# Kernel optimization log

Hardware: AMD Instinct MI355X
Metric: run time of the kernel (lower is better)

## Reference

```python
import jax, jax.numpy as jnp
import numpy as np

B, CIN, H, W = 8, 1, 192, 192
COUT, KH, KW = 8, 7, 7


def setup_inputs() -> dict:
    key = jax.random.key(0)
    k1, k2, k3 = jax.random.split(key, 3)
    x = jax.random.normal(k1, (B, CIN, H, W), dtype=jnp.float32)
    # original init: filter ~ N(0, 0.01), alpha = 0 (use small nonzero alpha)
    filt = 0.01 * jax.random.normal(k2, (COUT, CIN, KH, KW), dtype=jnp.float32)
    alpha = 0.1 * jax.random.normal(k3, (COUT, CIN), dtype=jnp.float32)
    return {"x": x, "filt": filt, "alpha": alpha}


def _smorph(x, filt, alpha):
    # x: [B, Cin, H, W]; filt: [Cout, Cin, kh, kw]; alpha: [Cout, Cin]
    b, cin, h, w = x.shape
    cout, _, kh, kw = filt.shape
    ho, wo = h - kh + 1, w - kw + 1  # 'valid' windowing as in _smorph_py
    # sliding-window patches: [B, Cin, kh*kw, Ho, Wo] (static slices, traced once)
    patches = jnp.stack(
        [x[:, :, ky:ky + ho, kx:kx + wo] for ky in range(kh) for kx in range(kw)],
        axis=2,
    )
    # s[b,co,ci,k,y,x] = input[b,ci,y+ky,x+kx] + filter[co,ci,ky,kx]
    s = patches[:, None] + filt.reshape(cout, cin, kh * kw, 1, 1)[None]
    a = alpha[None, :, :, None, None, None]  # broadcast over B, taps, space
    e = jnp.exp(a * s)
    num = jnp.sum(s * e, axis=(2, 3))  # sum over Cin and taps -> [B,Cout,Ho,Wo]
    den = jnp.sum(e, axis=(2, 3))
    return num / den


def reference(x, filt, alpha):
    # dual=False: single soft-morphology pass
    return _smorph(x, filt, alpha)
```

## Files before the change

### kernel.cpp

```cpp
#include <hip/hip_runtime.h>

#ifndef __has_builtin
#define __has_builtin(x) 0
#endif

__device__ __forceinline__ float fexp2(float v) {
#if __has_builtin(__builtin_amdgcn_exp2f)
    return __builtin_amdgcn_exp2f(v);
#else
    return exp2f(v);
#endif
}
__device__ __forceinline__ float frcp(float v) {
#if __has_builtin(__builtin_amdgcn_rcpf)
    return __builtin_amdgcn_rcpf(v);
#else
    return 1.0f / v;
#endif
}

constexpr int B_    = 8;
constexpr int H_    = 192;
constexpr int W_    = 192;
constexpr int COUT_ = 8;
constexpr int KH_   = 7;
constexpr int KW_   = 7;
constexpr int HO_   = H_ - KH_ + 1;
constexpr int WO_   = W_ - KW_ + 1;
constexpr float LOG2E = 1.44269504088896340736f;

constexpr int TX   = 64;
constexpr int TY   = 8;
constexpr int IX   = TX + KW_ - 1;
constexpr int IY   = TY + KH_ - 1;
constexpr int NPIX = IX * IY;

__global__ void smorph_setup(const float* __restrict__ filt,
                             const float* __restrict__ alpha,
                             float* __restrict__ ws) {
    int i = threadIdx.x;
    if (i < COUT_ * KH_) {
        int c = i / 7, ky = i - c * 7;
        float a2 = alpha[c] * LOG2E;
        float* t = ws + (c * 7 + ky) * 16;
#pragma unroll
        for (int kx = 0; kx < 7; ++kx) {
            float f = filt[(c * 7 + ky) * 7 + kx];
            float F = fexp2(a2 * f);
            t[kx]     = F;
            t[8 + kx] = F * f;
        }
        t[7] = 0.f; t[15] = 0.f;
    }
}

__global__ __launch_bounds__(256) void smorph_main(
    const float* __restrict__ x,
    const float* __restrict__ alpha,
    const float* __restrict__ fg,
    float* __restrict__ out)
{
    __shared__ __align__(16) float2 PH[IY * IX];

    const int tx  = threadIdx.x;
    const int ty  = threadIdx.y;
    const int tid = ty * 32 + tx;
    const int bx0 = blockIdx.x * TX;
    const int by0 = blockIdx.y * TY;
    const int z   = blockIdx.z;
    const int c   = z & 7;
    const float* xb = x + (z >> 3) * (H_ * W_);
    const float a2  = alpha[c] * LOG2E;

    const int i0 = tid, i1 = tid + 256, i2 = tid + 512, i3 = tid + 768;
    const int iy0 = i0 / IX, ix0 = i0 - iy0 * IX;
    const int iy1 = i1 / IX, ix1 = i1 - iy1 * IX;
    const int iy2 = i2 / IX, ix2 = i2 - iy2 * IX;
    const int iy3 = i3 / IX, ix3 = i3 - iy3 * IX;
    const bool has3 = (i3 < NPIX);

    const float xv0 = xb[min(by0 + iy0, H_ - 1) * W_ + min(bx0 + ix0, W_ - 1)];
    const float xv1 = xb[min(by0 + iy1, H_ - 1) * W_ + min(bx0 + ix1, W_ - 1)];
    const float xv2 = xb[min(by0 + iy2, H_ - 1) * W_ + min(bx0 + ix2, W_ - 1)];
    const float xv3 = has3 ? xb[min(by0 + iy3, H_ - 1) * W_ + min(bx0 + ix3, W_ - 1)] : 0.f;

    {
        float P;
        P = fexp2(a2 * xv0); PH[iy0 * IX + ix0] = make_float2(P, xv0 * P);
        P = fexp2(a2 * xv1); PH[iy1 * IX + ix1] = make_float2(P, xv1 * P);
        P = fexp2(a2 * xv2); PH[iy2 * IX + ix2] = make_float2(P, xv2 * P);
        if (has3) { P = fexp2(a2 * xv3); PH[iy3 * IX + ix3] = make_float2(P, xv3 * P); }
    }
    __syncthreads();

    const int ox = bx0 + 2 * tx;
    const int oy = by0 + ty;
    const bool valid = (ox + 1 < WO_) && (oy < HO_);

    float num0 = 0.f, den0 = 0.f, num1 = 0.f, den1 = 0.f;
    const float* tc = fg + c * (7 * 16);
#pragma unroll
    for (int ky = 0; ky < KH_; ++ky) {
        const float* t = tc + ky * 16;
        const float4* rp = (const float4*)&PH[(ty + ky) * IX + 2 * tx];
        float4 q0 = rp[0], q1 = rp[1], q2 = rp[2], q3 = rp[3];
        float P[8]  = {q0.x, q0.z, q1.x, q1.z, q2.x, q2.z, q3.x, q3.z};
        float Hh[8] = {q0.y, q0.w, q1.y, q1.w, q2.y, q2.w, q3.y, q3.w};
#pragma unroll
        for (int kx = 0; kx < 7; ++kx) {
            const float F = t[kx], G = t[8 + kx];
            num0 = fmaf(F, Hh[kx],     num0);
            num0 = fmaf(G, P[kx],      num0);
            den0 = fmaf(F, P[kx],      den0);
            num1 = fmaf(F, Hh[kx + 1], num1);
            num1 = fmaf(G, P[kx + 1],  num1);
            den1 = fmaf(F, P[kx + 1],  den1);
        }
    }

    if (valid) {
        float2 o;
        o.x = num0 * frcp(den0);
        o.y = num1 * frcp(den1);
        *(float2*)&out[(z * HO_ + oy) * WO_ + ox] = o;
    }
}

extern "C" void kernel_launch(void* const* d_in, const int* in_sizes, int n_in,
                              void* d_out, int out_size, void* d_ws, size_t ws_size,
                              hipStream_t stream) {
    const float* x     = (const float*)d_in[0];
    const float* filt  = (const float*)d_in[1];
    const float* alpha = (const float*)d_in[2];
    float* out = (float*)d_out;
    float* ws  = (float*)d_ws;

    smorph_setup<<<1, 64, 0, stream>>>(filt, alpha, ws);

    dim3 block(32, 8, 1);
    dim3 grid((WO_ + TX - 1) / TX, (HO_ + TY - 1) / TY, B_ * COUT_);
    smorph_main<<<grid, block, 0, stream>>>(x, alpha, ws, out);
}
```

Baseline: 73.98 us.

## Compute four output rows per thread with taller tiles to reuse LDS row loads

Raises the tile height from 8 to 32 rows so each thread computes a 4x2 output patch. Each shared-memory row is read once and applied to up to four output rows, which cuts LDS reads per output and shrinks the halo overhead per tile. In exchange it needs more registers for the accumulators and larger shared memory. It also launches fewer blocks, and the last row tile is partly wasted because 186 rows do not divide evenly by 32.

```diff
diff --git a/kernel.cpp b/kernel.cpp
--- a/kernel.cpp
+++ b/kernel.cpp
@@ -30,10 +30,11 @@
 constexpr float LOG2E = 1.44269504088896340736f;
 
 constexpr int TX   = 64;
-constexpr int TY   = 8;
+constexpr int TY   = 32;
 constexpr int IX   = TX + KW_ - 1;
 constexpr int IY   = TY + KH_ - 1;
 constexpr int NPIX = IX * IY;
+constexpr int NSLOT = (NPIX + 255) / 256;
 
 __global__ void smorph_setup(const float* __restrict__ filt,
                              const float* __restrict__ alpha,
@@ -72,57 +73,59 @@
     const float* xb = x + (z >> 3) * (H_ * W_);
     const float a2  = alpha[c] * LOG2E;
 
-    const int i0 = tid, i1 = tid + 256, i2 = tid + 512, i3 = tid + 768;
-    const int iy0 = i0 / IX, ix0 = i0 - iy0 * IX;
-    const int iy1 = i1 / IX, ix1 = i1 - iy1 * IX;
-    const int iy2 = i2 / IX, ix2 = i2 - iy2 * IX;
-    const int iy3 = i3 / IX, ix3 = i3 - iy3 * IX;
-    const bool has3 = (i3 < NPIX);
-
-    const float xv0 = xb[min(by0 + iy0, H_ - 1) * W_ + min(bx0 + ix0, W_ - 1)];
-    const float xv1 = xb[min(by0 + iy1, H_ - 1) * W_ + min(bx0 + ix1, W_ - 1)];
-    const float xv2 = xb[min(by0 + iy2, H_ - 1) * W_ + min(bx0 + ix2, W_ - 1)];
-    const float xv3 = has3 ? xb[min(by0 + iy3, H_ - 1) * W_ + min(bx0 + ix3, W_ - 1)] : 0.f;
-
-    {
-        float P;
-        P = fexp2(a2 * xv0); PH[iy0 * IX + ix0] = make_float2(P, xv0 * P);
-        P = fexp2(a2 * xv1); PH[iy1 * IX + ix1] = make_float2(P, xv1 * P);
-        P = fexp2(a2 * xv2); PH[iy2 * IX + ix2] = make_float2(P, xv2 * P);
-        if (has3) { P = fexp2(a2 * xv3); PH[iy3 * IX + ix3] = make_float2(P, xv3 * P); }
+#pragma unroll
+    for (int s = 0; s < NSLOT; ++s) {
+        const int i = tid + 256 * s;
+        if (i < NPIX) {
+            const int iy = i / IX, ix = i - iy * IX;
+            const float xv = xb[min(by0 + iy, H_ - 1) * W_ + min(bx0 + ix, W_ - 1)];
+            const float P = fexp2(a2 * xv);
+            PH[i] = make_float2(P, xv * P);
+        }
     }
     __syncthreads();
 
-    const int ox = bx0 + 2 * tx;
-    const int oy = by0 + ty;
-    const bool valid = (ox + 1 < WO_) && (oy < HO_);
+    const int ox  = bx0 + 2 * tx;
+    const int oyb = by0 + 4 * ty;
+    const bool vx = (ox + 1 < WO_);
 
-    float num0 = 0.f, den0 = 0.f, num1 = 0.f, den1 = 0.f;
+    float num[4][2] = {};
+    float den[4][2] = {};
     const float* tc = fg + c * (7 * 16);
+
 #pragma unroll
-    for (int ky = 0; ky < KH_; ++ky) {
-        const float* t = tc + ky * 16;
-        const float4* rp = (const float4*)&PH[(ty + ky) * IX + 2 * tx];
+    for (int ir = 0; ir < 4 + KH_ - 1; ++ir) {
+        const float4* rp = (const float4*)&PH[(4 * ty + ir) * IX + 2 * tx];
         float4 q0 = rp[0], q1 = rp[1], q2 = rp[2], q3 = rp[3];
         float P[8]  = {q0.x, q0.z, q1.x, q1.z, q2.x, q2.z, q3.x, q3.z};
         float Hh[8] = {q0.y, q0.w, q1.y, q1.w, q2.y, q2.w, q3.y, q3.w};
 #pragma unroll
-        for (int kx = 0; kx < 7; ++kx) {
-            const float F = t[kx], G = t[8 + kx];
-            num0 = fmaf(F, Hh[kx],     num0);
-            num0 = fmaf(G, P[kx],      num0);
-            den0 = fmaf(F, P[kx],      den0);
-            num1 = fmaf(F, Hh[kx + 1], num1);
-            num1 = fmaf(G, P[kx + 1],  num1);
-            den1 = fmaf(F, P[kx + 1],  den1);
+        for (int ro = 0; ro < 4; ++ro) {
+            const int ky = ir - ro;
+            if (ky < 0 || ky > KH_ - 1) continue;
+            const float* t = tc + ky * 16;
+#pragma unroll
+            for (int kx = 0; kx < 7; ++kx) {
+                const float F = t[kx], G = t[8 + kx];
+                num[ro][0] = fmaf(F, Hh[kx],     num[ro][0]);
+                num[ro][0] = fmaf(G, P[kx],      num[ro][0]);
+                den[ro][0] = fmaf(F, P[kx],      den[ro][0]);
+                num[ro][1] = fmaf(F, Hh[kx + 1], num[ro][1]);
+                num[ro][1] = fmaf(G, P[kx + 1],  num[ro][1]);
+                den[ro][1] = fmaf(F, P[kx + 1],  den[ro][1]);
+            }
         }
     }
 
-    if (valid) {
-        float2 o;
-        o.x = num0 * frcp(den0);
-        o.y = num1 * frcp(den1);
-        *(float2*)&out[(z * HO_ + oy) * WO_ + ox] = o;
+#pragma unroll
+    for (int ro = 0; ro < 4; ++ro) {
+        const int oy = oyb + ro;
+        if (vx && oy < HO_) {
+            float2 o;
+            o.x = num[ro][0] * frcp(den[ro][0]);
+            o.y = num[ro][1] * frcp(den[ro][1]);
+            *(float2*)&out[(z * HO_ + oy) * WO_ + ox] = o;
+        }
     }
 }
 
```

New measurement: 89.43 us. 1.21x slower.

## Shrink tile to 32x8 with 128-thread blocks and remap threads to rows

Applied to the files above, without the earlier changes.

Halves the tile width to 32 outputs and the block to 128 threads, with each thread covering two adjacent output columns. Threads are remapped so each 32-lane group handles two rows of 16 column pairs, and the launch bounds now request higher occupancy. The shared-memory load becomes a generic strided loop. Smaller tiles give more blocks, which should fill the GPU better and cut the tail for this small problem, at the cost of a larger halo overhead (38x14 inputs per 32x8 outputs).

```diff
diff --git a/kernel.cpp b/kernel.cpp
--- a/kernel.cpp
+++ b/kernel.cpp
@@ -29,11 +29,13 @@
 constexpr int WO_   = W_ - KW_ + 1;
 constexpr float LOG2E = 1.44269504088896340736f;
 
-constexpr int TX   = 64;
+constexpr int NTHR = 128;
+constexpr int TX   = 32;
 constexpr int TY   = 8;
 constexpr int IX   = TX + KW_ - 1;
 constexpr int IY   = TY + KH_ - 1;
 constexpr int NPIX = IX * IY;
+constexpr int NSLOT = (NPIX + NTHR - 1) / NTHR;
 
 __global__ void smorph_setup(const float* __restrict__ filt,
                              const float* __restrict__ alpha,
@@ -54,7 +56,7 @@
     }
 }
 
-__global__ __launch_bounds__(256) void smorph_main(
+__global__ __launch_bounds__(NTHR, 8) void smorph_main(
     const float* __restrict__ x,
     const float* __restrict__ alpha,
     const float* __restrict__ fg,
@@ -72,37 +74,30 @@
     const float* xb = x + (z >> 3) * (H_ * W_);
     const float a2  = alpha[c] * LOG2E;
 
-    const int i0 = tid, i1 = tid + 256, i2 = tid + 512, i3 = tid + 768;
-    const int iy0 = i0 / IX, ix0 = i0 - iy0 * IX;
-    const int iy1 = i1 / IX, ix1 = i1 - iy1 * IX;
-    const int iy2 = i2 / IX, ix2 = i2 - iy2 * IX;
-    const int iy3 = i3 / IX, ix3 = i3 - iy3 * IX;
-    const bool has3 = (i3 < NPIX);
-
-    const float xv0 = xb[min(by0 + iy0, H_ - 1) * W_ + min(bx0 + ix0, W_ - 1)];
-    const float xv1 = xb[min(by0 + iy1, H_ - 1) * W_ + min(bx0 + ix1, W_ - 1)];
-    const float xv2 = xb[min(by0 + iy2, H_ - 1) * W_ + min(bx0 + ix2, W_ - 1)];
-    const float xv3 = has3 ? xb[min(by0 + iy3, H_ - 1) * W_ + min(bx0 + ix3, W_ - 1)] : 0.f;
-
-    {
-        float P;
-        P = fexp2(a2 * xv0); PH[iy0 * IX + ix0] = make_float2(P, xv0 * P);
-        P = fexp2(a2 * xv1); PH[iy1 * IX + ix1] = make_float2(P, xv1 * P);
-        P = fexp2(a2 * xv2); PH[iy2 * IX + ix2] = make_float2(P, xv2 * P);
-        if (has3) { P = fexp2(a2 * xv3); PH[iy3 * IX + ix3] = make_float2(P, xv3 * P); }
+#pragma unroll
+    for (int s = 0; s < NSLOT; ++s) {
+        const int i = tid + NTHR * s;
+        if (i < NPIX) {
+            const int iy = i / IX, ix = i - iy * IX;
+            const float xv = xb[min(by0 + iy, H_ - 1) * W_ + min(bx0 + ix, W_ - 1)];
+            const float P = fexp2(a2 * xv);
+            PH[i] = make_float2(P, xv * P);
+        }
     }
     __syncthreads();
 
-    const int ox = bx0 + 2 * tx;
-    const int oy = by0 + ty;
-    const bool valid = (ox + 1 < WO_) && (oy < HO_);
+    const int xs = tx & 15;
+    const int yr = (ty << 1) | (tx >> 4);
+    const int ox = bx0 + 2 * xs;
+    const int oy = by0 + yr;
+    const bool vx = (ox + 1 < WO_);
 
     float num0 = 0.f, den0 = 0.f, num1 = 0.f, den1 = 0.f;
     const float* tc = fg + c * (7 * 16);
 #pragma unroll
     for (int ky = 0; ky < KH_; ++ky) {
         const float* t = tc + ky * 16;
-        const float4* rp = (const float4*)&PH[(ty + ky) * IX + 2 * tx];
+        const float4* rp = (const float4*)&PH[(yr + ky) * IX + 2 * xs];
         float4 q0 = rp[0], q1 = rp[1], q2 = rp[2], q3 = rp[3];
         float P[8]  = {q0.x, q0.z, q1.x, q1.z, q2.x, q2.z, q3.x, q3.z};
         float Hh[8] = {q0.y, q0.w, q1.y, q1.w, q2.y, q2.w, q3.y, q3.w};
@@ -118,7 +113,7 @@
         }
     }
 
-    if (valid) {
+    if (vx && oy < HO_) {
         float2 o;
         o.x = num0 * frcp(den0);
         o.y = num1 * frcp(den1);
@@ -137,7 +132,7 @@
 
     smorph_setup<<<1, 64, 0, stream>>>(filt, alpha, ws);
 
-    dim3 block(32, 8, 1);
+    dim3 block(32, 4, 1);
     dim3 grid((WO_ + TX - 1) / TX, (HO_ + TY - 1) / TY, B_ * COUT_);
     smorph_main<<<grid, block, 0, stream>>>(x, alpha, ws, out);
 }
```

After: 76.06 us. +2.8%, slower.
